# Performance work log

Hardware: AMD Instinct MI355X
Metric: run time of the kernel (lower is better)

Reference implementation:

```python
import jax, jax.numpy as jnp
import numpy as np

N = 100_000      # num_nodes
E = 3_200_000    # num_edges (avg degree 32)
F_IN = 8         # node_features
H = 64           # hidden_size
EPS = 1e-5       # batchnorm eps


def setup_inputs() -> dict:
    key = jax.random.key(0)
    ks = jax.random.split(key, 12)
    s = 0.05
    inp = {
        "x": jax.random.normal(ks[0], (N, F_IN), dtype=jnp.float32),
        "edge_index": jax.random.randint(ks[1], (2, E), 0, N, dtype=jnp.int32),
        "edge_weight": jax.random.uniform(ks[2], (E,), dtype=jnp.float32),
        # GCNConv 1: in -> hidden
        "W1": jax.random.normal(ks[3], (F_IN, H), dtype=jnp.float32) * s,
        "b1": jnp.zeros((H,), jnp.float32),
        # GCNConv 2: hidden -> hidden
        "W2": jax.random.normal(ks[4], (H, H), dtype=jnp.float32) * s,
        "b2": jnp.zeros((H,), jnp.float32),
        # BatchNorm1d (eval mode: running stats)
        "bn1_gamma": jnp.ones((H,), jnp.float32), "bn1_beta": jnp.zeros((H,), jnp.float32),
        "bn1_mean": jnp.zeros((H,), jnp.float32), "bn1_var": jnp.ones((H,), jnp.float32),
        "bn2_gamma": jnp.ones((H,), jnp.float32), "bn2_beta": jnp.zeros((H,), jnp.float32),
        "bn2_mean": jnp.zeros((H,), jnp.float32), "bn2_var": jnp.ones((H,), jnp.float32),
        # LSTM 1: input 2H -> hidden H (window=1, zero init state => W_hh contributes nothing)
        "Wih1": jax.random.normal(ks[5], (4 * H, 2 * H), jnp.float32) * s,
        "bih1": jnp.zeros((4 * H,), jnp.float32), "bhh1": jnp.zeros((4 * H,), jnp.float32),
        # LSTM 2: input H -> hidden H
        "Wih2": jax.random.normal(ks[6], (4 * H, H), jnp.float32) * s,
        "bih2": jnp.zeros((4 * H,), jnp.float32), "bhh2": jnp.zeros((4 * H,), jnp.float32),
        # final Linear(2H + F_IN -> 1)
        "Wlin": jax.random.normal(ks[7], (2 * H + F_IN, 1), jnp.float32) * s,
        "blin": jnp.zeros((1,), jnp.float32),
    }
    return inp


def _gcn_conv(x, src, dst, w, W, b):
    # PyG GCNConv: linear, then sym-normalized propagation with self-loops (weight 1), then bias.
    h = x @ W                                                   # [N, H]
    deg = jnp.zeros((N,), h.dtype).at[dst].add(w) + 1.0         # weighted in-degree + self-loop
    dinv = jax.lax.rsqrt(deg)
    norm = dinv[src] * w * dinv[dst]                            # [E]
    agg = jax.ops.segment_sum(norm[:, None] * h[src], dst, num_segments=N)
    agg = agg + h * (1.0 / deg)[:, None]                        # self-loop term (norm = 1/deg)
    return agg + b


def _bn_eval(x, gamma, beta, mean, var):
    return (x - mean) * jax.lax.rsqrt(var + EPS) * gamma + beta


def _lstm_step0(x, Wih, bih, bhh):
    # single LSTM step from (h0, c0) = 0; PyTorch gate order i, f, g, o
    g = x @ Wih.T + (bih + bhh)
    i, f, gg, o = jnp.split(g, 4, axis=1)
    c = jax.nn.sigmoid(i) * jnp.tanh(gg)
    return jax.nn.sigmoid(o) * jnp.tanh(c)


def reference(x, edge_index, edge_weight,
              W1, b1, W2, b2,
              bn1_gamma, bn1_beta, bn1_mean, bn1_var,
              bn2_gamma, bn2_beta, bn2_mean, bn2_var,
              Wih1, bih1, bhh1, Wih2, bih2, bhh2,
              Wlin, blin):
    src, dst = edge_index[0], edge_index[1]
    # MPNNLSTM (window=1, eval: dropout disabled, batchnorm uses running stats)
    h1 = _bn_eval(jax.nn.relu(_gcn_conv(x, src, dst, edge_weight, W1, b1)),
                  bn1_gamma, bn1_beta, bn1_mean, bn1_var)
    h2 = _bn_eval(jax.nn.relu(_gcn_conv(h1, src, dst, edge_weight, W2, b2)),
                  bn2_gamma, bn2_beta, bn2_mean, bn2_var)
    feats = jnp.concatenate([h1, h2], axis=1)                   # [N, 2H]
    lh1 = _lstm_step0(feats, Wih1, bih1, bhh1)                  # [N, H]
    lh2 = _lstm_step0(lh1, Wih2, bih2, bhh2)                    # [N, H]
    Hcat = jnp.concatenate([lh1, lh2, x], axis=1)               # [N, 2H + F_IN]  (S == x for window=1)
    return jax.nn.relu(Hcat) @ Wlin + blin                      # [N, 1]
```

## Files before the change

### kernel.cpp

```cpp
#include <hip/hip_runtime.h>

#define BN_EPS 1e-5f
#define CHUNK_SHIFT 14
#define CHUNK (1 << CHUNK_SHIFT)
#define RANGE 50176
#define WSCALE (1.0f / 32767.0f)

typedef __bf16 bf16x8 __attribute__((ext_vector_type(8)));
typedef float f32x4 __attribute__((ext_vector_type(4)));

__device__ __forceinline__ float sigf(float x) { return 1.0f / (1.0f + __expf(-x)); }
__device__ __forceinline__ float tanh_fast(float x) {
    float t = __expf(-2.0f * fabsf(x));
    float r = (1.0f - t) / (1.0f + t);
    return copysignf(r, x);
}

__global__ __launch_bounds__(256)
void k_hist(const int* __restrict__ ei, unsigned* __restrict__ histg,
            unsigned char* __restrict__ rloc, int E, int NP, int B) {
    __shared__ unsigned hist[RANGE / 4];
    int c = blockIdx.x % B;
    int r = blockIdx.x / B;
    int base = r * RANGE;
    for (int k = threadIdx.x; k < RANGE / 4; k += 256) hist[k] = 0;
    __syncthreads();
    int i0 = c << CHUNK_SHIFT;
    int iend = min(i0 + CHUNK, E);
    for (int i = i0 + (int)threadIdx.x; i < iend; i += 256) {
        int d = ei[E + i] - base;
        if ((unsigned)d < (unsigned)RANGE) {
            unsigned sh = (d & 3) * 8;
            unsigned old = atomicAdd(&hist[d >> 2], 1u << sh);
            rloc[i] = (unsigned char)((old >> sh) & 0xFFu);
        }
    }
    __syncthreads();
    unsigned* dstp = histg + ((size_t)c * NP + base) / 4;
    for (int k = threadIdx.x; k < RANGE / 4; k += 256) dstp[k] = hist[k];
}

__global__ void k_colscan(const unsigned char* __restrict__ histg,
                          unsigned char* __restrict__ pref, int* __restrict__ cnt,
                          int N, int NP, int B) {
    int d = blockIdx.x * 256 + threadIdx.x;
    if (d >= N) return;
    int acc = 0;
    for (int b = 0; b < B; ++b) {
        size_t idx = (size_t)b * NP + d;
        int v = histg[idx];
        pref[idx] = (unsigned char)acc;
        acc += v;
    }
    cnt[d] = acc;
}

__global__ void k_scanA(const int* __restrict__ cnt,
                        int* __restrict__ rowstart, int* __restrict__ bsum, int n) {
    __shared__ int ws[4];
    int tid = threadIdx.x;
    int i0 = blockIdx.x * 1024 + tid * 4;
    int v0 = (i0     < n) ? cnt[i0]     : 0;
    int v1 = (i0 + 1 < n) ? cnt[i0 + 1] : 0;
    int v2 = (i0 + 2 < n) ? cnt[i0 + 2] : 0;
    int v3 = (i0 + 3 < n) ? cnt[i0 + 3] : 0;
    int s = v0 + v1 + v2 + v3;
    int lane = tid & 63, wid = tid >> 6;
    int inc = s;
    #pragma unroll
    for (int off = 1; off < 64; off <<= 1) {
        int t = __shfl_up(inc, off, 64);
        if (lane >= off) inc += t;
    }
    if (lane == 63) ws[wid] = inc;
    __syncthreads();
    int wpref = 0;
    #pragma unroll
    for (int k = 0; k < 4; ++k) if (k < wid) wpref += ws[k];
    int excl = wpref + inc - s;
    if (i0     < n) rowstart[i0]     = excl;
    if (i0 + 1 < n) rowstart[i0 + 1] = excl + v0;
    if (i0 + 2 < n) rowstart[i0 + 2] = excl + v0 + v1;
    if (i0 + 3 < n) rowstart[i0 + 3] = excl + v0 + v1 + v2;
    if (tid == 255) bsum[blockIdx.x] = wpref + inc;
}

__global__ void k_scanB(int* __restrict__ bsum, int nchunk) {
    __shared__ int ws[4];
    int tid = threadIdx.x;
    int v = (tid < nchunk) ? bsum[tid] : 0;
    int lane = tid & 63, wid = tid >> 6;
    int inc = v;
    #pragma unroll
    for (int off = 1; off < 64; off <<= 1) {
        int t = __shfl_up(inc, off, 64);
        if (lane >= off) inc += t;
    }
    if (lane == 63) ws[wid] = inc;
    __syncthreads();
    int wpref = 0;
    #pragma unroll
    for (int k = 0; k < 4; ++k) if (k < wid) wpref += ws[k];
    if (tid < nchunk) bsum[tid] = wpref + inc - v;
    if (tid == 255) bsum[nchunk] = ws[0] + ws[1] + ws[2] + ws[3];
}

__global__ void k_scanC(int* __restrict__ rowstart, const int* __restrict__ bsum,
                        int n, int nchunk) {
    int i = blockIdx.x * 256 + threadIdx.x;
    if (i < n) rowstart[i] += bsum[i >> 10];
    if (i == 0) rowstart[n] = bsum[nchunk];
}

__global__ void k_fill(const int* __restrict__ ei, const float* __restrict__ w,
                       const int* __restrict__ rowstart,
                       const unsigned char* __restrict__ rloc,
                       const unsigned char* __restrict__ pref,
                       unsigned* __restrict__ csr, int E, int NP) {
    int i = blockIdx.x * 256 + threadIdx.x;
    if (i < E) {
        int s = ei[i], d = ei[E + i];
        int c = i >> CHUNK_SHIFT;
        int pos = rowstart[d] + (int)pref[(size_t)c * NP + d] + (int)rloc[i];
        unsigned q = (unsigned)(w[i] * 32767.0f + 0.5f);
        csr[pos] = (q << 17) | (unsigned)s;
    }
}

__global__ void k_rowsum(const unsigned* __restrict__ csr,
                         const int* __restrict__ rowstart,
                         float* __restrict__ dinv, float* __restrict__ invd, int N) {
    int lane = threadIdx.x & 63;
    int n = blockIdx.x * 4 + (threadIdx.x >> 6);
    if (n >= N) return;
    int e0 = rowstart[n], e1 = rowstart[n + 1];
    int qs = 0;
    for (int j = e0 + lane; j < e1; j += 64)
        qs += (int)(csr[j] >> 17);
    #pragma unroll
    for (int off = 32; off; off >>= 1) qs += __shfl_xor(qs, off, 64);
    if (lane == 0) {
        float d = (float)qs * WSCALE + 1.0f;
        dinv[n] = rsqrtf(d);
        invd[n] = 1.0f / d;
    }
}

__global__ void k_prep(const float* __restrict__ Wih1, const float* __restrict__ bih1,
                       const float* __restrict__ bhh1, const float* __restrict__ Wih2,
                       const float* __restrict__ bih2, const float* __restrict__ bhh2,
                       const float* __restrict__ W2,
                       __bf16* __restrict__ wb1, __bf16* __restrict__ wb2,
                       __bf16* __restrict__ w2t,
                       float* __restrict__ bias1, float* __restrict__ bias2) {
    int idx = blockIdx.x * 256 + threadIdx.x;
    if (idx < 192 * 128) {
        int r = idx >> 7, k = idx & 127;
        int orig = r + (r >= 64 ? 64 : 0);
        wb1[idx] = (__bf16)Wih1[orig * 128 + k];
    }
    if (idx < 192 * 64) {
        int r = idx >> 6, k = idx & 63;
        int orig = r + (r >= 64 ? 64 : 0);
        wb2[idx] = (__bf16)Wih2[orig * 64 + k];
    }
    if (idx < 64 * 64) {
        int f = idx >> 6, k = idx & 63;
        w2t[idx] = (__bf16)W2[k * 64 + f];
    }
    if (idx < 192) {
        int orig = idx + (idx >= 64 ? 64 : 0);
        bias1[idx] = bih1[orig] + bhh1[orig];
        bias2[idx] = bih2[orig] + bhh2[orig];
    }
}

__global__ void k_lin1(const float* __restrict__ x, const float* __restrict__ W1,
                       __bf16* __restrict__ out, int N) {
    __shared__ float sW[512];
    sW[threadIdx.x] = W1[threadIdx.x];
    sW[threadIdx.x + 256] = W1[threadIdx.x + 256];
    __syncthreads();
    int lane = threadIdx.x & 63;
    int n = blockIdx.x * 4 + (threadIdx.x >> 6);
    if (n >= N) return;
    const float* xr = x + n * 8;
    float acc = 0.f;
    #pragma unroll
    for (int k = 0; k < 8; ++k) acc = fmaf(xr[k], sW[k * 64 + lane], acc);
    out[(size_t)n * 64 + lane] = (__bf16)acc;
}

__global__ __launch_bounds__(256)
void k_lin2m(const __bf16* __restrict__ hb1, const __bf16* __restrict__ w2t,
             __bf16* __restrict__ h2linb, int N) {
    __shared__ __bf16 lds[64 * 72];
    int tid = threadIdx.x, lane = tid & 63, w = tid >> 6;
    int n0 = blockIdx.x * 64;
    int lr = lane & 15, lk = lane >> 4;

    f32x4 acc[4];
    #pragma unroll
    for (int mt = 0; mt < 4; ++mt) acc[mt] = (f32x4){0.f, 0.f, 0.f, 0.f};

    const __bf16* wbase = w2t + (w * 16 + lr) * 64 + lk * 8;
    #pragma unroll
    for (int ks = 0; ks < 2; ++ks) {
        int koff = ks * 32 + lk * 8;
        bf16x8 B = *(const bf16x8*)(wbase + ks * 32);
        #pragma unroll
        for (int mt = 0; mt < 4; ++mt) {
            int node = n0 + mt * 16 + lr;
            bf16x8 A = *(const bf16x8*)(hb1 + (size_t)node * 64 + koff);
            acc[mt] = __builtin_amdgcn_mfma_f32_16x16x32_bf16(A, B, acc[mt], 0, 0, 0);
        }
    }
    int h = w * 16 + lr;
    #pragma unroll
    for (int mt = 0; mt < 4; ++mt)
        #pragma unroll
        for (int r = 0; r < 4; ++r)
            lds[(mt * 16 + lk * 4 + r) * 72 + h] = (__bf16)acc[mt][r];
    __syncthreads();
    int row = tid >> 2, q = tid & 3;
    int node = n0 + row;
    if (node < N) {
        float4* dst = (float4*)(h2linb + (size_t)node * 64 + q * 16);
        const float4* s = (const float4*)(lds + row * 72 + q * 16);
        dst[0] = s[0];
        dst[1] = s[1];
    }
}

__global__ void k_agg(const __bf16* __restrict__ hlin, const float* __restrict__ dinv,
                      const float* __restrict__ invd,
                      const int* __restrict__ rowstart, const unsigned* __restrict__ csr,
                      const float* __restrict__ bias,
                      const float* __restrict__ gam, const float* __restrict__ bet,
                      const float* __restrict__ mu, const float* __restrict__ var,
                      __bf16* __restrict__ hb, int N) {
    int lane = threadIdx.x & 63;
    int n = blockIdx.x * 4 + (threadIdx.x >> 6);
    if (n >= N) return;
    float eacc = 0.f;
    int e0 = rowstart[n], e1 = rowstart[n + 1];
    int j = e0;
    for (; j + 4 <= e1; j += 4) {
        unsigned p0 = csr[j], p1 = csr[j + 1], p2 = csr[j + 2], p3 = csr[j + 3];
        int s0 = (int)(p0 & 0x1FFFFu), s1 = (int)(p1 & 0x1FFFFu);
        int s2 = (int)(p2 & 0x1FFFFu), s3 = (int)(p3 & 0x1FFFFu);
        float c0 = (float)(p0 >> 17) * dinv[s0];
        float c1 = (float)(p1 >> 17) * dinv[s1];
        float c2 = (float)(p2 >> 17) * dinv[s2];
        float c3 = (float)(p3 >> 17) * dinv[s3];
        float v0 = (float)hlin[(size_t)s0 * 64 + lane];
        float v1 = (float)hlin[(size_t)s1 * 64 + lane];
        float v2 = (float)hlin[(size_t)s2 * 64 + lane];
        float v3 = (float)hlin[(size_t)s3 * 64 + lane];
        eacc = fmaf(c0, v0, eacc);
        eacc = fmaf(c1, v1, eacc);
        eacc = fmaf(c2, v2, eacc);
        eacc = fmaf(c3, v3, eacc);
    }
    for (; j < e1; ++j) {
        unsigned p = csr[j];
        int s = (int)(p & 0x1FFFFu);
        eacc = fmaf((float)(p >> 17) * dinv[s],
                    (float)hlin[(size_t)s * 64 + lane], eacc);
    }
    float acc = (float)hlin[(size_t)n * 64 + lane] * invd[n]
              + eacc * dinv[n] * WSCALE;
    float v = fmaxf(acc + bias[lane], 0.f);
    v = (v - mu[lane]) * rsqrtf(var[lane] + BN_EPS) * gam[lane] + bet[lane];
    hb[(size_t)n * 64 + lane] = (__bf16)v;
}

__global__ __launch_bounds__(256)
void k_lstm1(const __bf16* __restrict__ h1b, const __bf16* __restrict__ h2b,
             const __bf16* __restrict__ wb, const float* __restrict__ bias,
             const float* __restrict__ Wlin,
             __bf16* __restrict__ lhb, float* __restrict__ out, int N) {
    __shared__ __bf16 lh_lds[64 * 72];
    __shared__ float pbuf[64][4];
    int tid = threadIdx.x;
    int lane = tid & 63;
    int w = tid >> 6;
    int n0 = blockIdx.x * 64;
    int lr = lane & 15;
    int lk = lane >> 4;

    f32x4 acc[3][4];
    #pragma unroll
    for (int g = 0; g < 3; ++g)
        #pragma unroll
        for (int mt = 0; mt < 4; ++mt) acc[g][mt] = (f32x4){0.f, 0.f, 0.f, 0.f};

    const __bf16* wbase = wb + (w * 16 + lr) * 128 + lk * 8;
    #pragma unroll
    for (int ks = 0; ks < 4; ++ks) {
        int koff = ks * 32 + lk * 8;
        const __bf16* fb = (koff < 64) ? (h1b + koff) : (h2b + (koff - 64));
        bf16x8 A[4];
        #pragma unroll
        for (int mt = 0; mt < 4; ++mt) {
            int node = n0 + mt * 16 + lr;
            A[mt] = *(const bf16x8*)(fb + (size_t)node * 64);
        }
        #pragma unroll
        for (int g = 0; g < 3; ++g) {
            bf16x8 B = *(const bf16x8*)(wbase + g * 64 * 128 + ks * 32);
            #pragma unroll
            for (int mt = 0; mt < 4; ++mt)
                acc[g][mt] = __builtin_amdgcn_mfma_f32_16x16x32_bf16(A[mt], B, acc[g][mt], 0, 0, 0);
        }
    }

    int h = w * 16 + lr;
    float bI = bias[h], bG = bias[64 + h], bO = bias[128 + h];
    #pragma unroll
    for (int mt = 0; mt < 4; ++mt) {
        #pragma unroll
        for (int r = 0; r < 4; ++r) {
            int nl = mt * 16 + lk * 4 + r;
            float iv = sigf(acc[0][mt][r] + bI);
            float gv = tanh_fast(acc[1][mt][r] + bG);
            float ov = sigf(acc[2][mt][r] + bO);
            float lh = ov * tanh_fast(iv * gv);
            lh_lds[nl * 72 + h] = (__bf16)lh;
        }
    }
    __syncthreads();

    int row = tid >> 2, q = tid & 3;
    const __bf16* lrow = lh_lds + row * 72 + q * 16;
    float p = 0.f;
    #pragma unroll
    for (int c = 0; c < 16; ++c) p = fmaf(fmaxf((float)lrow[c], 0.f), Wlin[q * 16 + c], p);
    pbuf[row][q] = p;
    int node = n0 + row;
    if (node < N) {
        float4* dst = (float4*)(lhb + (size_t)node * 64 + q * 16);
        const float4* s = (const float4*)lrow;
        dst[0] = s[0];
        dst[1] = s[1];
    }
    __syncthreads();
    if (tid < 64) {
        int nd = n0 + tid;
        if (nd < N)
            out[nd] = pbuf[tid][0] + pbuf[tid][1] + pbuf[tid][2] + pbuf[tid][3];
    }
}

__global__ __launch_bounds__(256)
void k_lstm2(const __bf16* __restrict__ lhb, const float* __restrict__ xg,
             const __bf16* __restrict__ wb, const float* __restrict__ bias,
             const float* __restrict__ Wlin, const float* __restrict__ blin,
             float* __restrict__ out, int N) {
    __shared__ __bf16 lh_lds[64 * 72];
    __shared__ float pbuf[64][4];
    int tid = threadIdx.x;
    int lane = tid & 63;
    int w = tid >> 6;
    int n0 = blockIdx.x * 64;
    int lr = lane & 15;
    int lk = lane >> 4;

    f32x4 acc[3][4];
    #pragma unroll
    for (int g = 0; g < 3; ++g)
        #pragma unroll
        for (int mt = 0; mt < 4; ++mt) acc[g][mt] = (f32x4){0.f, 0.f, 0.f, 0.f};

    const __bf16* wbase = wb + (w * 16 + lr) * 64 + lk * 8;
    #pragma unroll
    for (int ks = 0; ks < 2; ++ks) {
        int koff = ks * 32 + lk * 8;
        bf16x8 A[4];
        #pragma unroll
        for (int mt = 0; mt < 4; ++mt) {
            int node = n0 + mt * 16 + lr;
            A[mt] = *(const bf16x8*)(lhb + (size_t)node * 64 + koff);
        }
        #pragma unroll
        for (int g = 0; g < 3; ++g) {
            bf16x8 B = *(const bf16x8*)(wbase + g * 64 * 64 + ks * 32);
            #pragma unroll
            for (int mt = 0; mt < 4; ++mt)
                acc[g][mt] = __builtin_amdgcn_mfma_f32_16x16x32_bf16(A[mt], B, acc[g][mt], 0, 0, 0);
        }
    }

    int h = w * 16 + lr;
    float bI = bias[h], bG = bias[64 + h], bO = bias[128 + h];
    #pragma unroll
    for (int mt = 0; mt < 4; ++mt) {
        #pragma unroll
        for (int r = 0; r < 4; ++r) {
            int nl = mt * 16 + lk * 4 + r;
            float iv = sigf(acc[0][mt][r] + bI);
            float gv = tanh_fast(acc[1][mt][r] + bG);
            float ov = sigf(acc[2][mt][r] + bO);
            float lh = ov * tanh_fast(iv * gv);
            lh_lds[nl * 72 + h] = (__bf16)lh;
        }
    }
    __syncthreads();

    int row = tid >> 2, q = tid & 3;
    const __bf16* lrow = lh_lds + row * 72 + q * 16;
    float p = 0.f;
    #pragma unroll
    for (int c = 0; c < 16; ++c) p = fmaf(fmaxf((float)lrow[c], 0.f), Wlin[64 + q * 16 + c], p);
    pbuf[row][q] = p;
    __syncthreads();
    if (tid < 64) {
        int nd = n0 + tid;
        if (nd < N) {
            float o = out[nd] + blin[0] + pbuf[tid][0] + pbuf[tid][1] + pbuf[tid][2] + pbuf[tid][3];
            const float* xr = xg + (size_t)nd * 8;
            #pragma unroll
            for (int k = 0; k < 8; ++k) o = fmaf(fmaxf(xr[k], 0.f), Wlin[128 + k], o);
            out[nd] = o;
        }
    }
}

extern "C" void kernel_launch(void* const* d_in, const int* in_sizes, int n_in,
                              void* d_out, int out_size, void* d_ws, size_t ws_size,
                              hipStream_t stream) {
    const float* x    = (const float*)d_in[0];
    const int*   ei   = (const int*)d_in[1];
    const float* ew   = (const float*)d_in[2];
    const float* W1   = (const float*)d_in[3];
    const float* b1   = (const float*)d_in[4];
    const float* W2   = (const float*)d_in[5];
    const float* b2   = (const float*)d_in[6];
    const float* bn1g = (const float*)d_in[7];
    const float* bn1b = (const float*)d_in[8];
    const float* bn1m = (const float*)d_in[9];
    const float* bn1v = (const float*)d_in[10];
    const float* bn2g = (const float*)d_in[11];
    const float* bn2b = (const float*)d_in[12];
    const float* bn2m = (const float*)d_in[13];
    const float* bn2v = (const float*)d_in[14];
    const float* Wih1 = (const float*)d_in[15];
    const float* bih1 = (const float*)d_in[16];
    const float* bhh1 = (const float*)d_in[17];
    const float* Wih2 = (const float*)d_in[18];
    const float* bih2 = (const float*)d_in[19];
    const float* bhh2 = (const float*)d_in[20];
    const float* Wlin = (const float*)d_in[21];
    const float* blin = (const float*)d_in[22];
    float* out = (float*)d_out;

    int N = in_sizes[0] / 8;
    int E = in_sizes[2];

    int B  = (E + CHUNK - 1) >> CHUNK_SHIFT;
    int NR = (N + RANGE - 1) / RANGE;
    int NP = NR * RANGE;
    int nchunk = (N + 1023) / 1024;

    char* ws = (char*)d_ws;
    size_t off = 0;
    auto alloc = [&](size_t bytes) -> void* {
        void* p = ws + off;
        off = (off + bytes + 255) & ~(size_t)255;
        return p;
    };
    unsigned* histg          = (unsigned*)alloc((size_t)B * NP);
    unsigned char* pref      = (unsigned char*)alloc((size_t)B * NP);
    unsigned char* rloc      = (unsigned char*)alloc((size_t)E);
    int*   cnt      = (int*)alloc((size_t)N * 4);
    float* dinv     = (float*)alloc((size_t)N * 4);
    float* invd     = (float*)alloc((size_t)N * 4);
    int*   rowstart = (int*)alloc((size_t)(N + 1) * 4);
    int*   bsum     = (int*)alloc((size_t)(nchunk + 1) * 4);
    unsigned* csr   = (unsigned*)alloc((size_t)E * 4);
    __bf16* h1linb  = (__bf16*)alloc((size_t)N * 64 * 2);
    __bf16* hb1     = (__bf16*)alloc((size_t)N * 64 * 2);
    __bf16* h2linb  = (__bf16*)alloc((size_t)N * 64 * 2);
    __bf16* hb2     = (__bf16*)alloc((size_t)N * 64 * 2);
    __bf16* lhb     = (__bf16*)alloc((size_t)N * 64 * 2);
    __bf16* wb1     = (__bf16*)alloc((size_t)192 * 128 * 2);
    __bf16* wb2     = (__bf16*)alloc((size_t)192 * 64 * 2);
    __bf16* w2t     = (__bf16*)alloc((size_t)64 * 64 * 2);
    float* bias1    = (float*)alloc(192 * 4);
    float* bias2    = (float*)alloc(192 * 4);

    const int tb = 256;
    int gE = (E + tb - 1) / tb;
    int gN = (N + tb - 1) / tb;
    int nb4 = (N + 3) / 4;
    int nT = (N + 63) / 64;

    k_prep<<<96, tb, 0, stream>>>(Wih1, bih1, bhh1, Wih2, bih2, bhh2, W2,
                                  wb1, wb2, w2t, bias1, bias2);
    k_hist<<<B * NR, tb, 0, stream>>>(ei, histg, rloc, E, NP, B);
    k_colscan<<<gN, tb, 0, stream>>>((const unsigned char*)histg, pref, cnt, N, NP, B);
    k_scanA<<<nchunk, tb, 0, stream>>>(cnt, rowstart, bsum, N);
    k_scanB<<<1, tb, 0, stream>>>(bsum, nchunk);
    k_scanC<<<gN, tb, 0, stream>>>(rowstart, bsum, N, nchunk);
    k_fill<<<gE, tb, 0, stream>>>(ei, ew, rowstart, rloc, pref, csr, E, NP);
    k_rowsum<<<nb4, tb, 0, stream>>>(csr, rowstart, dinv, invd, N);

    k_lin1<<<nb4, tb, 0, stream>>>(x, W1, h1linb, N);
    k_agg<<<nb4, tb, 0, stream>>>(h1linb, dinv, invd, rowstart, csr,
                                  b1, bn1g, bn1b, bn1m, bn1v, hb1, N);
    k_lin2m<<<nT, tb, 0, stream>>>(hb1, w2t, h2linb, N);
    k_agg<<<nb4, tb, 0, stream>>>(h2linb, dinv, invd, rowstart, csr,
                                  b2, bn2g, bn2b, bn2m, bn2v, hb2, N);

    k_lstm1<<<nT, tb, 0, stream>>>(hb1, hb2, wb1, bias1, Wlin, lhb, out, N);
    k_lstm2<<<nT, tb, 0, stream>>>(lhb, x, wb2, bias2, Wlin, blin, out, N);
}
```

Measured before the change: 464.4 us.

## Split GCN aggregation into four 16-feature slabs for cache-friendly gathers

The linear outputs are now stored as four feature-slab tables of 16 features each ([4][N][16] bf16) instead of [N][64]. Aggregation runs four passes, one per slab. Within a pass, each wave handles one node with 4 edge groups × 16 features and combines the groups with cross-lane shuffles. The aim is a smaller gathered working set per pass (3.2 MB per slab), so random neighbor gathers hit in L2/MALL more often. The cost is four times as many CSR and dinv reads and that each wave writes only 16 outputs.

```diff
diff --git a/kernel.cpp b/kernel.cpp
--- a/kernel.cpp
+++ b/kernel.cpp
@@ -176,7 +176,7 @@
 }
 
 __global__ void k_lin1(const float* __restrict__ x, const float* __restrict__ W1,
-                       __bf16* __restrict__ out, int N) {
+                       __bf16* __restrict__ out_s, int N) {
     __shared__ float sW[512];
     sW[threadIdx.x] = W1[threadIdx.x];
     sW[threadIdx.x + 256] = W1[threadIdx.x + 256];
@@ -188,12 +188,12 @@
     float acc = 0.f;
     #pragma unroll
     for (int k = 0; k < 8; ++k) acc = fmaf(xr[k], sW[k * 64 + lane], acc);
-    out[(size_t)n * 64 + lane] = (__bf16)acc;
+    out_s[((size_t)(lane >> 4) * N + n) * 16 + (lane & 15)] = (__bf16)acc;
 }
 
 __global__ __launch_bounds__(256)
 void k_lin2m(const __bf16* __restrict__ hb1, const __bf16* __restrict__ w2t,
-             __bf16* __restrict__ h2linb, int N) {
+             __bf16* __restrict__ h2s, int N) {
     __shared__ __bf16 lds[64 * 72];
     int tid = threadIdx.x, lane = tid & 63, w = tid >> 6;
     int n0 = blockIdx.x * 64;
@@ -225,54 +225,53 @@
     int row = tid >> 2, q = tid & 3;
     int node = n0 + row;
     if (node < N) {
-        float4* dst = (float4*)(h2linb + (size_t)node * 64 + q * 16);
+        float4* dst = (float4*)(h2s + ((size_t)q * N + node) * 16);
         const float4* s = (const float4*)(lds + row * 72 + q * 16);
         dst[0] = s[0];
         dst[1] = s[1];
     }
 }
 
-__global__ void k_agg(const __bf16* __restrict__ hlin, const float* __restrict__ dinv,
-                      const float* __restrict__ invd,
-                      const int* __restrict__ rowstart, const unsigned* __restrict__ csr,
-                      const float* __restrict__ bias,
-                      const float* __restrict__ gam, const float* __restrict__ bet,
-                      const float* __restrict__ mu, const float* __restrict__ var,
-                      __bf16* __restrict__ hb, int N) {
-    int lane = threadIdx.x & 63;
-    int n = blockIdx.x * 4 + (threadIdx.x >> 6);
+__global__ __launch_bounds__(256)
+void k_agg_fs(const __bf16* __restrict__ hs, const float* __restrict__ dinv,
+              const float* __restrict__ invd,
+              const int* __restrict__ rowstart, const unsigned* __restrict__ csr,
+              const float* __restrict__ bias,
+              const float* __restrict__ gam, const float* __restrict__ bet,
+              const float* __restrict__ mu, const float* __restrict__ var,
+              __bf16* __restrict__ hb, int N, int nbw) {
+    int tid = threadIdx.x;
+    int lane = tid & 63;
+    int g = lane >> 4, f = lane & 15;
+    int pass = blockIdx.x / nbw;
+    int n = (blockIdx.x % nbw) * 4 + (tid >> 6);
     if (n >= N) return;
+    const __bf16* tab = hs + (size_t)pass * N * 16;
+    int e0 = rowstart[n], e1 = rowstart[n + 1];
     float eacc = 0.f;
-    int e0 = rowstart[n], e1 = rowstart[n + 1];
-    int j = e0;
-    for (; j + 4 <= e1; j += 4) {
-        unsigned p0 = csr[j], p1 = csr[j + 1], p2 = csr[j + 2], p3 = csr[j + 3];
+    int j = e0 + g;
+    for (; j + 4 < e1; j += 8) {
+        unsigned p0 = csr[j], p1 = csr[j + 4];
         int s0 = (int)(p0 & 0x1FFFFu), s1 = (int)(p1 & 0x1FFFFu);
-        int s2 = (int)(p2 & 0x1FFFFu), s3 = (int)(p3 & 0x1FFFFu);
+        float v0 = (float)tab[(size_t)s0 * 16 + f];
+        float v1 = (float)tab[(size_t)s1 * 16 + f];
         float c0 = (float)(p0 >> 17) * dinv[s0];
         float c1 = (float)(p1 >> 17) * dinv[s1];
-        float c2 = (float)(p2 >> 17) * dinv[s2];
-        float c3 = (float)(p3 >> 17) * dinv[s3];
-        float v0 = (float)hlin[(size_t)s0 * 64 + lane];
-        float v1 = (float)hlin[(size_t)s1 * 64 + lane];
-        float v2 = (float)hlin[(size_t)s2 * 64 + lane];
-        float v3 = (float)hlin[(size_t)s3 * 64 + lane];
         eacc = fmaf(c0, v0, eacc);
         eacc = fmaf(c1, v1, eacc);
-        eacc = fmaf(c2, v2, eacc);
-        eacc = fmaf(c3, v3, eacc);
-    }
-    for (; j < e1; ++j) {
+    }
+    if (j < e1) {
         unsigned p = csr[j];
         int s = (int)(p & 0x1FFFFu);
-        eacc = fmaf((float)(p >> 17) * dinv[s],
-                    (float)hlin[(size_t)s * 64 + lane], eacc);
-    }
-    float acc = (float)hlin[(size_t)n * 64 + lane] * invd[n]
-              + eacc * dinv[n] * WSCALE;
-    float v = fmaxf(acc + bias[lane], 0.f);
-    v = (v - mu[lane]) * rsqrtf(var[lane] + BN_EPS) * gam[lane] + bet[lane];
-    hb[(size_t)n * 64 + lane] = (__bf16)v;
+        eacc = fmaf((float)(p >> 17) * dinv[s], (float)tab[(size_t)s * 16 + f], eacc);
+    }
+    eacc += __shfl_xor(eacc, 16, 64);
+    eacc += __shfl_xor(eacc, 32, 64);
+    int fg = pass * 16 + f;
+    float acc = (float)tab[(size_t)n * 16 + f] * invd[n] + eacc * dinv[n] * WSCALE;
+    float v = fmaxf(acc + bias[fg], 0.f);
+    v = (v - mu[fg]) * rsqrtf(var[fg] + BN_EPS) * gam[fg] + bet[fg];
+    if (g == 0) hb[(size_t)n * 64 + fg] = (__bf16)v;
 }
 
 __global__ __launch_bounds__(256)
@@ -478,9 +477,9 @@
     int*   rowstart = (int*)alloc((size_t)(N + 1) * 4);
     int*   bsum     = (int*)alloc((size_t)(nchunk + 1) * 4);
     unsigned* csr   = (unsigned*)alloc((size_t)E * 4);
-    __bf16* h1linb  = (__bf16*)alloc((size_t)N * 64 * 2);
+    __bf16* h1s     = (__bf16*)alloc((size_t)N * 64 * 2);
     __bf16* hb1     = (__bf16*)alloc((size_t)N * 64 * 2);
-    __bf16* h2linb  = (__bf16*)alloc((size_t)N * 64 * 2);
+    __bf16* h2s     = (__bf16*)alloc((size_t)N * 64 * 2);
     __bf16* hb2     = (__bf16*)alloc((size_t)N * 64 * 2);
     __bf16* lhb     = (__bf16*)alloc((size_t)N * 64 * 2);
     __bf16* wb1     = (__bf16*)alloc((size_t)192 * 128 * 2);
@@ -494,6 +493,7 @@
     int gN = (N + tb - 1) / tb;
     int nb4 = (N + 3) / 4;
     int nT = (N + 63) / 64;
+    int nbw = (N + 3) / 4;
 
     k_prep<<<96, tb, 0, stream>>>(Wih1, bih1, bhh1, Wih2, bih2, bhh2, W2,
                                   wb1, wb2, w2t, bias1, bias2);
@@ -505,12 +505,12 @@
     k_fill<<<gE, tb, 0, stream>>>(ei, ew, rowstart, rloc, pref, csr, E, NP);
     k_rowsum<<<nb4, tb, 0, stream>>>(csr, rowstart, dinv, invd, N);
 
-    k_lin1<<<nb4, tb, 0, stream>>>(x, W1, h1linb, N);
-    k_agg<<<nb4, tb, 0, stream>>>(h1linb, dinv, invd, rowstart, csr,
-                                  b1, bn1g, bn1b, bn1m, bn1v, hb1, N);
-    k_lin2m<<<nT, tb, 0, stream>>>(hb1, w2t, h2linb, N);
-    k_agg<<<nb4, tb, 0, stream>>>(h2linb, dinv, invd, rowstart, csr,
-                                  b2, bn2g, bn2b, bn2m, bn2v, hb2, N);
+    k_lin1<<<nb4, tb, 0, stream>>>(x, W1, h1s, N);
+    k_agg_fs<<<nbw * 4, tb, 0, stream>>>(h1s, dinv, invd, rowstart, csr,
+                                         b1, bn1g, bn1b, bn1m, bn1v, hb1, N, nbw);
+    k_lin2m<<<nT, tb, 0, stream>>>(hb1, w2t, h2s, N);
+    k_agg_fs<<<nbw * 4, tb, 0, stream>>>(h2s, dinv, invd, rowstart, csr,
+                                         b2, bn2g, bn2b, bn2m, bn2v, hb2, N, nbw);
 
     k_lstm1<<<nT, tb, 0, stream>>>(hb1, hb2, wb1, bias1, Wlin, lhb, out, N);
     k_lstm2<<<nT, tb, 0, stream>>>(lhb, x, wb2, bias2, Wlin, blin, out, N);
```

Measured after the change: 690.3 us. 48.6% more time.
